# Kernel tuning notes

Measured on AMD Instinct MI355X. Metric: run time of the kernel, lower is better.

The kernel has to match this reference:

```python
import jax, jax.numpy as jnp
import numpy as np

B = 1024
EMB_DIM = 128      # channels fed to VQ; each channel's 5*5=25 spatial vector is one token
CODEBOOK = 1024
COMMIT = 0.25


def conv2d(x, w, b, pad=1):
    y = jax.lax.conv_general_dilated(x, w, (1, 1), [(pad, pad), (pad, pad)],
                                     dimension_numbers=('NCHW', 'OIHW', 'NCHW'))
    return y + b[None, :, None, None]


def maxpool2x2(x):
    b, c, h, w = x.shape
    xr = x.reshape(b, c, h // 2, 2, w // 2, 2).transpose(0, 1, 2, 4, 3, 5).reshape(b, c, h // 2, w // 2, 4)
    return jnp.max(xr, axis=-1), jnp.argmax(xr, axis=-1)


def maxunpool2x2(x, idx):
    b, c, h, w = x.shape
    y = x[..., None] * jax.nn.one_hot(idx, 4, dtype=x.dtype)
    return y.reshape(b, c, h, w, 2, 2).transpose(0, 1, 2, 4, 3, 5).reshape(b, c, h * 2, w * 2)


def setup_inputs() -> dict:
    key = jax.random.key(0)
    ks = jax.random.split(key, 12)
    f32 = jnp.float32

    def he(k, shape, fan_in):
        return jax.random.normal(k, shape, f32) * (2.0 / fan_in) ** 0.5

    return {
        'x': jax.random.normal(ks[0], (B, 3, 20, 20), f32),
        'enc1_w': he(ks[1], (32, 3, 3, 3), 27), 'enc1_b': jnp.zeros((32,), f32),
        'enc2_w': he(ks[2], (96, 32, 3, 3), 288), 'enc2_b': jnp.zeros((96,), f32),
        'pre_w': he(ks[3], (EMB_DIM, 96, 1, 1), 96), 'pre_b': jnp.zeros((EMB_DIM,), f32),
        'codebook': jax.random.normal(ks[4], (CODEBOOK, 25), f32),
        'trans_w': he(ks[5], (EMB_DIM, 96, 1, 1), EMB_DIM), 'trans_b': jnp.zeros((96,), f32),
        'dec1_w': he(ks[6], (32, 96, 3, 3), 864), 'dec1_b': jnp.zeros((32,), f32),
        'dec2_w': he(ks[7], (3, 32, 3, 3), 288), 'dec2_b': jnp.zeros((3,), f32),
        'hpe_w1': he(ks[8], (2400, 32), 2400), 'hpe_b1': jnp.zeros((32,), f32),
        'hpe_w2': he(ks[9], (32, 36), 32), 'hpe_b2': jnp.zeros((36,), f32),
    }


def reference(x, enc1_w, enc1_b, enc2_w, enc2_b, pre_w, pre_b, codebook,
              trans_w, trans_b, dec1_w, dec1_b, dec2_w, dec2_b,
              hpe_w1, hpe_b1, hpe_w2, hpe_b2):
    bsz = x.shape[0]
    # ---- Encoder: conv+relu+pool x2, keeping pool argmax indices ----
    h1 = jax.nn.relu(conv2d(x, enc1_w, enc1_b))          # [B,32,20,20]
    p1, idx1 = maxpool2x2(h1)                            # [B,32,10,10]
    h2 = jax.nn.relu(conv2d(p1, enc2_w, enc2_b))         # [B,96,10,10]
    z, idx2 = maxpool2x2(h2)                             # [B,96,5,5]
    # ---- pre-VQ 1x1 conv, tokens are per-channel 25-dim spatial vectors ----
    vq = conv2d(z, pre_w, pre_b, pad=0).reshape(bsz, -1, 25)   # [B,EMB_DIM,25]
    flat = vq.reshape(-1, 25)
    # squared L2 distances to codebook, argmin quantization
    d = (jnp.sum(flat * flat, -1, keepdims=True)
         - 2.0 * flat @ codebook.T
         + jnp.sum(codebook * codebook, -1))             # [B*EMB_DIM, CODEBOOK]
    indices = jnp.argmin(d, axis=-1).reshape(bsz, -1)    # [B,EMB_DIM]
    quantized = codebook[indices]                        # [B,EMB_DIM,25] gather
    vq_loss = COMMIT * jnp.mean((jax.lax.stop_gradient(quantized) - vq) ** 2)
    # unreliable_mode == 2 -> noisy_indices = indices (identity path)
    z_rec = codebook[indices].reshape(bsz, -1, 5, 5)     # [B,EMB_DIM,5,5]
    # ---- ConvTranspose2d 1x1 (torch weight layout [in,out,1,1]) ----
    latent = jnp.einsum('bihw,io->bohw', z_rec, trans_w[:, :, 0, 0]) + trans_b[None, :, None, None]
    # ---- Decoder: unpool(idx2)+conv+relu, unpool(idx1)+conv ----
    u2 = maxunpool2x2(latent, idx2)                      # [B,96,10,10]
    d1 = jax.nn.relu(conv2d(u2, dec1_w, dec1_b))         # [B,32,10,10]
    u1 = maxunpool2x2(d1, idx1)                          # [B,32,20,20]
    r_x = conv2d(u1, dec2_w, dec2_b)                     # [B,3,20,20]
    # ---- pose head on flattened latent (2400 = 96*5*5) ----
    feat = latent.reshape(bsz, -1)
    kp = jax.nn.relu(feat @ hpe_w1 + hpe_b1) @ hpe_w2 + hpe_b2
    return vq_loss, r_x, kp.reshape(bsz, -1, 2)
```

## Files before the change

kernel.cpp:

```cpp
#include <hip/hip_runtime.h>

typedef unsigned char u8;
typedef unsigned long long u64;
typedef _Float16 h2 __attribute__((ext_vector_type(2)));

__device__ inline h2 h2bits(unsigned int u) { union { unsigned int u; h2 h; } c; c.u = u; return c.h; }
__device__ inline unsigned int bitsh2(h2 h) { union { unsigned int u; h2 h; } c; c.h = h; return c.u; }
__device__ inline unsigned int f2hbits(float v) {
    union { _Float16 h; unsigned short u; } c; c.h = (_Float16)v; return (unsigned int)c.u;
}

#if __has_builtin(__builtin_amdgcn_fdot2)
__device__ inline float fdot2(h2 a, h2 b, float c) { return __builtin_amdgcn_fdot2(a, b, c, false); }
#else
__device__ inline float fdot2(h2 a, h2 b, float c) {
    return c + (float)a.x * (float)b.x + (float)a.y * (float)b.y;
}
#endif

__global__ __launch_bounds__(256) void k0t(const float* __restrict__ cb,
                                           float* __restrict__ cnorm,
                                           float* __restrict__ lossacc,
                                           const float* __restrict__ e2w,
                                           float* __restrict__ wT2,
                                           const float* __restrict__ d1w,
                                           unsigned int* __restrict__ wH6u,
                                           const float* __restrict__ d2w,
                                           unsigned int* __restrict__ wH7u) {
    int g = blockIdx.x * 256 + threadIdx.x;
    if (g < 1024) {
        float s = 0.f;
#pragma unroll
        for (int d = 0; d < 25; ++d) { float v = cb[g * 25 + d]; s += v * v; }
        cnorm[g] = s;
    }
    if (g == 0) lossacc[0] = 0.f;
    for (int i = g; i < 27648; i += 8192) {
        int oc = i / 288, r = i % 288, ci = r / 9, k = r % 9;
        wT2[((ci * 3 + k / 3) * 96 + oc) * 3 + (k % 3)] = e2w[i];
    }
    for (int i = g; i < 13824; i += 8192) {
        int oc = i & 31, r = i >> 5;
        int kx = r % 3, r2 = r / 3, ky = r2 % 3, cp = r2 / 3;
        float a = d1w[(oc * 96 + 2 * cp) * 9 + ky * 3 + kx];
        float b = d1w[(oc * 96 + 2 * cp + 1) * 9 + ky * 3 + kx];
        h2 v; v.x = (_Float16)a; v.y = (_Float16)b;
        wH6u[i] = bitsh2(v);
    }
    if (g < 432) {
        int oc = g % 3, r = g / 3;
        int kx = r % 3, r2 = r / 3, ky = r2 % 3, cp = r2 / 3;
        float a = d2w[(oc * 32 + 2 * cp) * 9 + ky * 3 + kx];
        float b = d2w[(oc * 32 + 2 * cp + 1) * 9 + ky * 3 + kx];
        h2 v; v.x = (_Float16)a; v.y = (_Float16)b;
        wH7u[g] = bitsh2(v);
    }
}

__global__ __launch_bounds__(128) void k1_enc1(const float* __restrict__ x,
                                               const float* __restrict__ w,
                                               const float* __restrict__ bias,
                                               float* __restrict__ p1,
                                               u64* __restrict__ idx1p) {
    const int img = blockIdx.x;
    const int tid = threadIdx.x;
    __shared__ __align__(16) float xs[1320];
    __shared__ float wss[864];
    __shared__ float bss[32];
    for (int i = tid; i < 1320; i += 128) xs[i] = 0.f;
    for (int i = tid; i < 864; i += 128) wss[i] = w[i];
    if (tid < 32) bss[tid] = bias[tid];
    __syncthreads();
    for (int i = tid; i < 1200; i += 128) {
        int ci = i / 400, s = i % 400, y = s / 20, xx = s % 20;
        xs[ci * 440 + y * 22 + xx + 1] = x[img * 1200 + i];
    }
    __syncthreads();
    if (tid >= 100) return;
    const int r = tid / 10, c = tid % 10;
    int ry[4]; bool mv[4];
#pragma unroll
    for (int wy = 0; wy < 4; ++wy) {
        int yy = 2 * r - 1 + wy;
        mv[wy] = (yy >= 0) && (yy <= 19);
        ry[wy] = min(max(yy, 0), 19);
    }
    u64 idxbits = 0;
    for (int ocg = 0; ocg < 4; ++ocg) {
        float acc[8][4];
#pragma unroll
        for (int j = 0; j < 8; ++j) {
            float bb = bss[ocg * 8 + j];
#pragma unroll
            for (int q = 0; q < 4; ++q) acc[j][q] = bb;
        }
        for (int ci = 0; ci < 3; ++ci) {
            float win[4][4];
#pragma unroll
            for (int wy = 0; wy < 4; ++wy)
#pragma unroll
                for (int wx = 0; wx < 4; ++wx) {
                    float v = xs[ci * 440 + ry[wy] * 22 + 2 * c + wx];
                    win[wy][wx] = mv[wy] ? v : 0.f;
                }
#pragma unroll
            for (int j = 0; j < 8; ++j) {
                const float* wr = &wss[((ocg * 8 + j) * 3 + ci) * 9];
#pragma unroll
                for (int q = 0; q < 4; ++q) {
                    int dr = q >> 1, dc = q & 1;
#pragma unroll
                    for (int ky = 0; ky < 3; ++ky)
#pragma unroll
                        for (int kx = 0; kx < 3; ++kx)
                            acc[j][q] = fmaf(win[dr + ky][dc + kx], wr[ky * 3 + kx], acc[j][q]);
                }
            }
        }
#pragma unroll
        for (int j = 0; j < 8; ++j) {
            int oc = ocg * 8 + j;
            float best = -1.f; int bi = 0;
#pragma unroll
            for (int q = 0; q < 4; ++q) {
                float v = fmaxf(acc[j][q], 0.f);
                if (v > best) { best = v; bi = q; }
            }
            p1[img * 3200 + oc * 100 + tid] = best;
            idxbits |= (u64)bi << (2 * oc);
        }
    }
    idx1p[img * 100 + tid] = idxbits;
}

__global__ __launch_bounds__(256) void k2f(const float* __restrict__ p1,
                                           const float* __restrict__ wT2,
                                           const float* __restrict__ bias,
                                           const float* __restrict__ prw,
                                           const float* __restrict__ prb,
                                           float* __restrict__ vqb,
                                           u8* __restrict__ idx2) {
    const int img = blockIdx.x;
    const int tid = threadIdx.x;
    __shared__ __align__(16) float up[4608];
    __shared__ __align__(16) float wch[6912];
    for (int i = tid; i < 4608; i += 256) up[i] = 0.f;
    __syncthreads();
    for (int i = tid; i < 3200; i += 256) {
        int ci = i / 100, s = i % 100;
        up[ci * 144 + (s / 10 + 1) * 12 + (s % 10) + 1] = p1[img * 3200 + i];
    }
    const int wv = tid >> 6;
    const int l  = tid & 63;
    const int ocsub = (l >= 25) ? 1 : 0;
    const int pos = l - ocsub * 25;
    const bool act = (l < 50);
    const int oc0 = wv * 24 + ocsub * 12;
    const int r = pos / 5, c = pos % 5;
    float acc[12][4];
#pragma unroll
    for (int j = 0; j < 12; ++j)
#pragma unroll
        for (int q = 0; q < 4; ++q) acc[j][q] = 0.f;
    for (int chunk = 0; chunk < 4; ++chunk) {
        __syncthreads();
        for (int i = tid; i < 6912; i += 256) wch[i] = wT2[chunk * 6912 + i];
        __syncthreads();
        if (act) {
            for (int cil = 0; cil < 8; ++cil) {
                const int base = (chunk * 8 + cil) * 144;
                float win[4][4];
#pragma unroll
                for (int wy = 0; wy < 4; ++wy) {
                    float2 a = *(const float2*)&up[base + (2 * r + wy) * 12 + 2 * c];
                    float2 b = *(const float2*)&up[base + (2 * r + wy) * 12 + 2 * c + 2];
                    win[wy][0] = a.x; win[wy][1] = a.y; win[wy][2] = b.x; win[wy][3] = b.y;
                }
#pragma unroll
                for (int ky = 0; ky < 3; ++ky) {
                    const float* wk = &wch[(cil * 3 + ky) * 288 + oc0 * 3];
                    float wreg[36];
#pragma unroll
                    for (int i4 = 0; i4 < 9; ++i4)
                        *(float4*)(wreg + 4 * i4) = *(const float4*)(wk + 4 * i4);
#pragma unroll
                    for (int j = 0; j < 12; ++j)
#pragma unroll
                        for (int q = 0; q < 4; ++q) {
                            int dr = q >> 1, dc = q & 1;
#pragma unroll
                            for (int kx = 0; kx < 3; ++kx)
                                acc[j][q] = fmaf(win[dr + ky][dc + kx], wreg[j * 3 + kx], acc[j][q]);
                        }
                }
            }
        }
    }
    float* zs = wch;
    float* wst = &wch[2688];
    __syncthreads();
    if (act) {
#pragma unroll
        for (int j = 0; j < 12; ++j) {
            int oc = oc0 + j;
            float bb = bias[oc];
            float best = -1.f; int bi = 0;
#pragma unroll
            for (int q = 0; q < 4; ++q) {
                float v = fmaxf(acc[j][q] + bb, 0.f);
                if (v > best) { best = v; bi = q; }
            }
            zs[oc * 28 + pos] = best;
            idx2[img * 2400 + oc * 25 + pos] = (u8)bi;
        }
    }
    __syncthreads();
    const int e = tid >> 1, sh = tid & 1;
    const int s0 = sh * 12, ns = sh ? 13 : 12;
    float acc2[13];
    {
        float bb = prb[e];
#pragma unroll
        for (int k = 0; k < 13; ++k) acc2[k] = bb;
    }
    for (int cc = 0; cc < 3; ++cc) {
        __syncthreads();
        for (int i = tid; i < 4096; i += 256)
            wst[(i >> 5) * 33 + (i & 31)] = prw[(i >> 5) * 96 + cc * 32 + (i & 31)];
        __syncthreads();
        for (int cil = 0; cil < 32; ++cil) {
            int ci = cc * 32 + cil;
            float wvv = wst[e * 33 + cil];
            float cz[16];
#pragma unroll
            for (int i4 = 0; i4 < 4; ++i4)
                *(float4*)(cz + 4 * i4) = *(const float4*)&zs[ci * 28 + s0 + 4 * i4];
#pragma unroll
            for (int k = 0; k < 13; ++k) acc2[k] = fmaf(wvv, cz[k], acc2[k]);
        }
    }
    float* ob = up;
#pragma unroll
    for (int k = 0; k < 13; ++k)
        if (k < ns) ob[e * 25 + s0 + k] = acc2[k];
    __syncthreads();
    for (int i = tid; i < 3200; i += 256) vqb[img * 3200 + i] = ob[i];
}

__global__ __launch_bounds__(256) void k3b_vq2(const float* __restrict__ vq,
                                               const float* __restrict__ cb,
                                               const float* __restrict__ cnorm,
                                               float* __restrict__ pbest,
                                               int* __restrict__ pbk) {
    const int tg = blockIdx.x >> 3;
    const int ch = blockIdx.x & 7;
    const int tid = threadIdx.x;
    const int k0 = ch * 128;
    __shared__ __align__(16) float cs[128 * 28];
    for (int i = tid; i < 128 * 28; i += 256) {
        int k = i / 28, d = i % 28;
        float v = 0.f;
        if (d < 25) v = cb[(k0 + k) * 25 + d];
        else if (d == 25) v = cnorm[k0 + k];
        cs[i] = v;
    }
    const int t0 = tg * 1024 + tid * 4;
    float f2[4][25];
#pragma unroll
    for (int t = 0; t < 4; ++t)
#pragma unroll
        for (int d = 0; d < 25; ++d)
            f2[t][d] = -2.f * vq[(t0 + t) * 25 + d];
    __syncthreads();
    float best[4] = {1e30f, 1e30f, 1e30f, 1e30f};
    int bk[4] = {0, 0, 0, 0};
    for (int k = 0; k < 128; ++k) {
        const float* crow = &cs[k * 28];
        float cc[28];
#pragma unroll
        for (int i = 0; i < 7; ++i)
            *(float4*)(cc + 4 * i) = *(const float4*)(crow + 4 * i);
        const float cn = cc[25];
        const int kg = k0 + k;
#pragma unroll
        for (int t = 0; t < 4; ++t) {
            float a = cn;
#pragma unroll
            for (int d = 0; d < 25; ++d) a = fmaf(f2[t][d], cc[d], a);
            if (a < best[t]) { best[t] = a; bk[t] = kg; }
        }
    }
#pragma unroll
    for (int t = 0; t < 4; ++t) {
        pbest[ch * 131072 + t0 + t] = best[t];
        pbk[ch * 131072 + t0 + t] = bk[t];
    }
}

__global__ __launch_bounds__(256) void k3r_reduce(const float* __restrict__ pbest,
                                                  const int* __restrict__ pbk,
                                                  const float* __restrict__ vq,
                                                  int* __restrict__ vqidx,
                                                  float* __restrict__ lossacc) {
    const int t = blockIdx.x * 256 + threadIdx.x;
    float best = 1e30f; int bk = 0;
#pragma unroll
    for (int ch = 0; ch < 8; ++ch) {
        float s = pbest[ch * 131072 + t];
        int k = pbk[ch * 131072 + t];
        if (s < best) { best = s; bk = k; }
    }
    vqidx[t] = bk;
    float fn = 0.f;
#pragma unroll
    for (int d = 0; d < 25; ++d) { float v = vq[t * 25 + d]; fn = fmaf(v, v, fn); }
    float dloc = fn + best;
#pragma unroll
    for (int off = 32; off > 0; off >>= 1) dloc += __shfl_down(dloc, off, 64);
    __shared__ float wsum[4];
    if ((threadIdx.x & 63) == 0) wsum[threadIdx.x >> 6] = dloc;
    __syncthreads();
    if (threadIdx.x == 0)
        atomicAdd(lossacc, wsum[0] + wsum[1] + wsum[2] + wsum[3]);
}

__global__ void kf_loss(const float* __restrict__ lossacc, float* __restrict__ out) {
    out[0] = 0.25f * lossacc[0] / 3276800.0f;
}

__global__ __launch_bounds__(256) void k5_latent_pose(
    const int* __restrict__ vqidx, const float* __restrict__ cb,
    const float* __restrict__ tw, const float* __restrict__ tbb,
    const float* __restrict__ w1, const float* __restrict__ b1,
    const float* __restrict__ w2, const float* __restrict__ b2,
    float* __restrict__ latg, float* __restrict__ outkp) {
    const int img = blockIdx.x;
    const int tid = threadIdx.x;
    __shared__ int idxs[128];
    __shared__ float zr[128 * 26];
    __shared__ float lat[2400];
    __shared__ float ps[256];
    __shared__ float hs[32];
    if (tid < 128) idxs[tid] = vqidx[img * 128 + tid];
    __syncthreads();
    for (int i = tid; i < 3200; i += 256) {
        int e = i / 25, d = i % 25;
        zr[e * 26 + d] = cb[idxs[e] * 25 + d];
    }
    __syncthreads();
    const int sg = tid % 5, og = tid / 5;
    if (og < 24) {
        const int oc0 = og * 4, s0 = sg * 5;
        float acc[4][5];
#pragma unroll
        for (int j = 0; j < 4; ++j)
#pragma unroll
            for (int ss = 0; ss < 5; ++ss) acc[j][ss] = 0.f;
        for (int e = 0; e < 128; ++e) {
            float zv[5];
#pragma unroll
            for (int ss = 0; ss < 5; ++ss) zv[ss] = zr[e * 26 + s0 + ss];
#pragma unroll
            for (int j = 0; j < 4; ++j) {
                float wv = tw[e * 96 + oc0 + j];
#pragma unroll
                for (int ss = 0; ss < 5; ++ss) acc[j][ss] += wv * zv[ss];
            }
        }
#pragma unroll
        for (int j = 0; j < 4; ++j) {
            float bb = tbb[oc0 + j];
#pragma unroll
            for (int ss = 0; ss < 5; ++ss) {
                float v = acc[j][ss] + bb;
                lat[(oc0 + j) * 25 + s0 + ss] = v;
                latg[img * 2400 + (oc0 + j) * 25 + s0 + ss] = v;
            }
        }
    }
    __syncthreads();
    {
        const int seg = tid >> 5, jj = tid & 31;
        float s = 0.f;
        const int i0 = seg * 300;
        for (int i = i0; i < i0 + 300; ++i) s += lat[i] * w1[i * 32 + jj];
        ps[seg * 32 + jj] = s;
    }
    __syncthreads();
    if (tid < 32) {
        float h = b1[tid];
#pragma unroll
        for (int s2 = 0; s2 < 8; ++s2) h += ps[s2 * 32 + tid];
        hs[tid] = fmaxf(h, 0.f);
    }
    __syncthreads();
    if (tid < 36) {
        float kp = b2[tid];
#pragma unroll
        for (int m = 0; m < 32; ++m) kp += hs[m] * w2[m * 36 + tid];
        outkp[img * 36 + tid] = kp;
    }
}

__global__ __launch_bounds__(128) void k6_dec1(const float* __restrict__ latg,
                                               const u8* __restrict__ idx2,
                                               const unsigned int* __restrict__ wH6,
                                               const float* __restrict__ bias,
                                               unsigned short* __restrict__ d1h) {
    const int img0 = blockIdx.x * 2;
    const int tid = threadIdx.x;
    __shared__ __align__(16) unsigned int uph[13824];
    __shared__ unsigned int wcs[2304];
    for (int i = tid; i < 13824; i += 128) uph[i] = 0u;
    __syncthreads();
    for (int g = tid; g < 2400; g += 128) {
        int m = g / 1200, r2 = g % 1200;
        int cp = r2 / 25, s = r2 % 25;
        int rr = (img0 + m) * 2400 + cp * 50 + s;
        int q0 = idx2[rr], q1 = idx2[rr + 25];
        float v0 = latg[rr], v1 = latg[rr + 25];
        unsigned int wq[4] = {0u, 0u, 0u, 0u};
        wq[q0] |= f2hbits(v0);
        wq[q1] |= f2hbits(v1) << 16;
        int pr = s / 5, pc = s % 5;
        int wb = m * 6912 + (cp * 12 + 2 * pr + 1) * 12 + 2 * pc + 1;
        uph[wb]      = wq[0];
        uph[wb + 1]  = wq[1];
        uph[wb + 12] = wq[2];
        uph[wb + 13] = wq[3];
    }
    const int m = tid >> 6;
    const int l = tid & 63;
    const int oc = l & 31, ys = l >> 5;
    float acc[50];
#pragma unroll
    for (int i = 0; i < 50; ++i) acc[i] = 0.f;
    for (int chunk = 0; chunk < 6; ++chunk) {
        __syncthreads();
        for (int i = tid; i < 2304; i += 128) wcs[i] = wH6[chunk * 2304 + i];
        __syncthreads();
        for (int cpl = 0; cpl < 8; ++cpl) {
            const int base = m * 6912 + (chunk * 8 + cpl) * 144 + ys * 60;
            unsigned int row[7][12];
#pragma unroll
            for (int k = 0; k < 7; ++k) {
                const uint4* rp = (const uint4*)&uph[base + k * 12];
                uint4 a = rp[0], b = rp[1], cc = rp[2];
                row[k][0] = a.x;  row[k][1] = a.y;  row[k][2] = a.z;  row[k][3] = a.w;
                row[k][4] = b.x;  row[k][5] = b.y;  row[k][6] = b.z;  row[k][7] = b.w;
                row[k][8] = cc.x; row[k][9] = cc.y; row[k][10] = cc.z; row[k][11] = cc.w;
            }
            h2 w9[9];
#pragma unroll
            for (int t = 0; t < 9; ++t) w9[t] = h2bits(wcs[(cpl * 9 + t) * 32 + oc]);
#pragma unroll
            for (int r = 0; r < 5; ++r)
#pragma unroll
                for (int j = 0; j < 10; ++j) {
                    float a = acc[r * 10 + j];
#pragma unroll
                    for (int ky = 0; ky < 3; ++ky)
#pragma unroll
                        for (int kx = 0; kx < 3; ++kx)
                            a = fdot2(h2bits(row[r + ky][j + kx]), w9[ky * 3 + kx], a);
                    acc[r * 10 + j] = a;
                }
        }
    }
    const float bb = bias[oc];
#pragma unroll
    for (int r = 0; r < 5; ++r)
#pragma unroll
        for (int j = 0; j < 10; ++j)
            d1h[(img0 + m) * 3200 + ((ys * 5 + r) * 10 + j) * 32 + oc] =
                (unsigned short)f2hbits(fmaxf(acc[r * 10 + j] + bb, 0.f));
}

__global__ __launch_bounds__(256) void k7_dec2(const unsigned int* __restrict__ d1w32,
                                               const u64* __restrict__ idx1p,
                                               const unsigned int* __restrict__ wH7,
                                               const float* __restrict__ bias,
                                               float* __restrict__ rx) {
    const int img = blockIdx.x;
    const int tid = threadIdx.x;
    __shared__ __align__(16) unsigned int uph[7040];
    __shared__ unsigned int wcs[448];
    for (int i = tid; i < 7040; i += 256) uph[i] = 0u;
    for (int i = tid; i < 448; i += 256) {
        int cp = i / 28, rr = i % 28;
        wcs[i] = (rr < 27) ? wH7[cp * 27 + rr] : 0u;
    }
    __syncthreads();
    for (int g = tid; g < 1600; g += 256) {
        int pos = g >> 4, cp = g & 15;
        unsigned int word = d1w32[img * 1600 + g];
        u64 bits = idx1p[img * 100 + pos];
        int q0 = (int)((bits >> (4 * cp)) & 3ull);
        int q1 = (int)((bits >> (4 * cp + 2)) & 3ull);
        unsigned int wq[4] = {0u, 0u, 0u, 0u};
        wq[q0] |= word & 0xFFFFu;
        wq[q1] |= word & 0xFFFF0000u;
        int r = pos / 10, c = pos % 10;
        int wb = cp * 440 + (2 * r) * 22 + 2 * c + 1;
        uph[wb]      = wq[0];
        uph[wb + 1]  = wq[1];
        uph[wb + 22] = wq[2];
        uph[wb + 23] = wq[3];
    }
    __syncthreads();
    if (tid >= 200) return;
    const int y = tid / 10, xp = tid % 10, x0 = 2 * xp;
    const bool m0 = (y > 0), m2 = (y < 19);
    const int ry0 = max(y - 1, 0), ry2 = min(y + 1, 19);
    float acc[3][2] = {{0.f, 0.f}, {0.f, 0.f}, {0.f, 0.f}};
    for (int cp = 0; cp < 16; ++cp) {
        const int base = cp * 440;
        unsigned int row[3][4];
        {
            uint2 a = *(const uint2*)&uph[base + ry0 * 22 + x0];
            uint2 b = *(const uint2*)&uph[base + ry0 * 22 + x0 + 2];
            row[0][0] = m0 ? a.x : 0u; row[0][1] = m0 ? a.y : 0u;
            row[0][2] = m0 ? b.x : 0u; row[0][3] = m0 ? b.y : 0u;
            a = *(const uint2*)&uph[base + y * 22 + x0];
            b = *(const uint2*)&uph[base + y * 22 + x0 + 2];
            row[1][0] = a.x; row[1][1] = a.y; row[1][2] = b.x; row[1][3] = b.y;
            a = *(const uint2*)&uph[base + ry2 * 22 + x0];
            b = *(const uint2*)&uph[base + ry2 * 22 + x0 + 2];
            row[2][0] = m2 ? a.x : 0u; row[2][1] = m2 ? a.y : 0u;
            row[2][2] = m2 ? b.x : 0u; row[2][3] = m2 ? b.y : 0u;
        }
#pragma unroll
        for (int oc = 0; oc < 3; ++oc)
#pragma unroll
            for (int ky = 0; ky < 3; ++ky)
#pragma unroll
                for (int kx = 0; kx < 3; ++kx) {
                    h2 wk = h2bits(wcs[cp * 28 + (ky * 3 + kx) * 3 + oc]);
                    acc[oc][0] = fdot2(h2bits(row[ky][kx]),     wk, acc[oc][0]);
                    acc[oc][1] = fdot2(h2bits(row[ky][kx + 1]), wk, acc[oc][1]);
                }
    }
#pragma unroll
    for (int oc = 0; oc < 3; ++oc)
#pragma unroll
        for (int dx = 0; dx < 2; ++dx)
            rx[img * 1200 + oc * 400 + y * 20 + x0 + dx] = acc[oc][dx] + bias[oc];
}

extern "C" void kernel_launch(void* const* d_in, const int* in_sizes, int n_in,
                              void* d_out, int out_size, void* d_ws, size_t ws_size,
                              hipStream_t stream) {
    const float* x   = (const float*)d_in[0];
    const float* e1w = (const float*)d_in[1];
    const float* e1b = (const float*)d_in[2];
    const float* e2w = (const float*)d_in[3];
    const float* e2b = (const float*)d_in[4];
    const float* prw = (const float*)d_in[5];
    const float* prb = (const float*)d_in[6];
    const float* cb  = (const float*)d_in[7];
    const float* tw  = (const float*)d_in[8];
    const float* tbb = (const float*)d_in[9];
    const float* d1w = (const float*)d_in[10];
    const float* d1b = (const float*)d_in[11];
    const float* d2w = (const float*)d_in[12];
    const float* d2b = (const float*)d_in[13];
    const float* hw1 = (const float*)d_in[14];
    const float* hb1 = (const float*)d_in[15];
    const float* hw2 = (const float*)d_in[16];
    const float* hb2 = (const float*)d_in[17];
    float* out = (float*)d_out;

    float* ws      = (float*)d_ws;
    float* cnorm   = ws;
    float* lossacc = cnorm + 1024;
    float* wT2     = lossacc + 4;
    unsigned int* wH6u = (unsigned int*)(wT2 + 27648);
    unsigned int* wH7u = wH6u + 13824;
    float* p1      = wT2 + 27648 + 27648;
    float* z       = p1 + 3276800;
    float* vq      = z + 2457600;
    int*   vqidx   = (int*)(vq + 3276800);
    u64*   idx1p   = (u64*)(vqidx + 131072);
    u8*    idx2    = (u8*)(idx1p + 102400);
    float* latent  = p1;
    unsigned short* d1h = (unsigned short*)vq;
    float* pbest   = z;
    int*   pbk     = (int*)(z + 1048576);

    float* rx  = out + 1;
    float* okp = out + 1 + 1228800;

    k0t<<<32, 256, 0, stream>>>(cb, cnorm, lossacc, e2w, wT2, d1w, wH6u, d2w, wH7u);
    k1_enc1<<<1024, 128, 0, stream>>>(x, e1w, e1b, p1, idx1p);
    k2f<<<1024, 256, 0, stream>>>(p1, wT2, e2b, prw, prb, vq, idx2);
    k3b_vq2<<<1024, 256, 0, stream>>>(vq, cb, cnorm, pbest, pbk);
    k3r_reduce<<<512, 256, 0, stream>>>(pbest, pbk, vq, vqidx, lossacc);
    kf_loss<<<1, 1, 0, stream>>>(lossacc, out);
    k5_latent_pose<<<1024, 256, 0, stream>>>(vqidx, cb, tw, tbb, hw1, hb1, hw2, hb2,
                                             latent, okp);
    k6_dec1<<<512, 128, 0, stream>>>(latent, idx2, wH6u, d1b, d1h);
    k7_dec2<<<1024, 256, 0, stream>>>((const unsigned int*)d1h, idx1p, wH7u, d2b, rx);
}
```

Baseline: 443.7 us.

## Process more images per block in enc2 and dec1 to amortize weight staging

k2f now handles two images per 512-thread block, sharing each staged weight chunk across both images and reusing the shared buffers for the projection stage. k6_dec1 handles four images per 256-thread block, staging the unpooled input in two channel halves so the shared footprint stays the same while each weight chunk load serves four images. The aim is to cut redundant global-to-LDS weight traffic and barrier overhead per image. In exchange the grids get smaller and k2f uses more LDS per block, which may lower occupancy.

```diff
diff --git a/kernel.cpp b/kernel.cpp
--- a/kernel.cpp
+++ b/kernel.cpp
@@ -133,29 +133,32 @@
     idx1p[img * 100 + tid] = idxbits;
 }
 
-__global__ __launch_bounds__(256) void k2f(const float* __restrict__ p1,
+__global__ __launch_bounds__(512) void k2f(const float* __restrict__ p1,
                                            const float* __restrict__ wT2,
                                            const float* __restrict__ bias,
                                            const float* __restrict__ prw,
                                            const float* __restrict__ prb,
                                            float* __restrict__ vqb,
                                            u8* __restrict__ idx2) {
-    const int img = blockIdx.x;
+    const int img0 = blockIdx.x * 2;
     const int tid = threadIdx.x;
-    __shared__ __align__(16) float up[4608];
+    __shared__ __align__(16) float up[9216];
     __shared__ __align__(16) float wch[6912];
-    for (int i = tid; i < 4608; i += 256) up[i] = 0.f;
-    __syncthreads();
-    for (int i = tid; i < 3200; i += 256) {
-        int ci = i / 100, s = i % 100;
-        up[ci * 144 + (s / 10 + 1) * 12 + (s % 10) + 1] = p1[img * 3200 + i];
+    for (int i = tid; i < 9216; i += 512) up[i] = 0.f;
+    __syncthreads();
+    for (int i = tid; i < 6400; i += 512) {
+        int m = i / 3200, r = i % 3200;
+        int ci = r / 100, s = r % 100;
+        up[m * 4608 + ci * 144 + (s / 10 + 1) * 12 + (s % 10) + 1] = p1[(img0 + m) * 3200 + r];
     }
     const int wv = tid >> 6;
+    const int m  = wv >> 2;
+    const int wvl = wv & 3;
     const int l  = tid & 63;
     const int ocsub = (l >= 25) ? 1 : 0;
     const int pos = l - ocsub * 25;
     const bool act = (l < 50);
-    const int oc0 = wv * 24 + ocsub * 12;
+    const int oc0 = wvl * 24 + ocsub * 12;
     const int r = pos / 5, c = pos % 5;
     float acc[12][4];
 #pragma unroll
@@ -164,11 +167,11 @@
         for (int q = 0; q < 4; ++q) acc[j][q] = 0.f;
     for (int chunk = 0; chunk < 4; ++chunk) {
         __syncthreads();
-        for (int i = tid; i < 6912; i += 256) wch[i] = wT2[chunk * 6912 + i];
+        for (int i = tid; i < 6912; i += 512) wch[i] = wT2[chunk * 6912 + i];
         __syncthreads();
         if (act) {
             for (int cil = 0; cil < 8; ++cil) {
-                const int base = (chunk * 8 + cil) * 144;
+                const int base = m * 4608 + (chunk * 8 + cil) * 144;
                 float win[4][4];
 #pragma unroll
                 for (int wy = 0; wy < 4; ++wy) {
@@ -197,7 +200,6 @@
         }
     }
     float* zs = wch;
-    float* wst = &wch[2688];
     __syncthreads();
     if (act) {
 #pragma unroll
@@ -210,12 +212,15 @@
                 float v = fmaxf(acc[j][q] + bb, 0.f);
                 if (v > best) { best = v; bi = q; }
             }
-            zs[oc * 28 + pos] = best;
-            idx2[img * 2400 + oc * 25 + pos] = (u8)bi;
-        }
-    }
-    __syncthreads();
-    const int e = tid >> 1, sh = tid & 1;
+            zs[m * 2688 + oc * 28 + pos] = best;
+            idx2[(img0 + m) * 2400 + oc * 25 + pos] = (u8)bi;
+        }
+    }
+    __syncthreads();
+    float* wst = up;
+    const int m2 = tid >> 8;
+    const int rr = tid & 255;
+    const int e = rr >> 1, sh = rr & 1;
     const int s0 = sh * 12, ns = sh ? 13 : 12;
     float acc2[13];
     {
@@ -225,7 +230,7 @@
     }
     for (int cc = 0; cc < 3; ++cc) {
         __syncthreads();
-        for (int i = tid; i < 4096; i += 256)
+        for (int i = tid; i < 4096; i += 512)
             wst[(i >> 5) * 33 + (i & 31)] = prw[(i >> 5) * 96 + cc * 32 + (i & 31)];
         __syncthreads();
         for (int cil = 0; cil < 32; ++cil) {
@@ -234,17 +239,18 @@
             float cz[16];
 #pragma unroll
             for (int i4 = 0; i4 < 4; ++i4)
-                *(float4*)(cz + 4 * i4) = *(const float4*)&zs[ci * 28 + s0 + 4 * i4];
+                *(float4*)(cz + 4 * i4) = *(const float4*)&zs[m2 * 2688 + ci * 28 + s0 + 4 * i4];
 #pragma unroll
             for (int k = 0; k < 13; ++k) acc2[k] = fmaf(wvv, cz[k], acc2[k]);
         }
     }
-    float* ob = up;
+    __syncthreads();
+    float* ob = wch;
 #pragma unroll
     for (int k = 0; k < 13; ++k)
-        if (k < ns) ob[e * 25 + s0 + k] = acc2[k];
-    __syncthreads();
-    for (int i = tid; i < 3200; i += 256) vqb[img * 3200 + i] = ob[i];
+        if (k < ns) ob[m2 * 3200 + e * 25 + s0 + k] = acc2[k];
+    __syncthreads();
+    for (int i = tid; i < 6400; i += 512) vqb[img0 * 3200 + i] = ob[i];
 }
 
 __global__ __launch_bounds__(256) void k3b_vq2(const float* __restrict__ vq,
@@ -402,69 +408,73 @@
     }
 }
 
-__global__ __launch_bounds__(128) void k6_dec1(const float* __restrict__ latg,
+__global__ __launch_bounds__(256) void k6_dec1(const float* __restrict__ latg,
                                                const u8* __restrict__ idx2,
                                                const unsigned int* __restrict__ wH6,
                                                const float* __restrict__ bias,
                                                unsigned short* __restrict__ d1h) {
-    const int img0 = blockIdx.x * 2;
+    const int img0 = blockIdx.x * 4;
     const int tid = threadIdx.x;
     __shared__ __align__(16) unsigned int uph[13824];
     __shared__ unsigned int wcs[2304];
-    for (int i = tid; i < 13824; i += 128) uph[i] = 0u;
-    __syncthreads();
-    for (int g = tid; g < 2400; g += 128) {
-        int m = g / 1200, r2 = g % 1200;
-        int cp = r2 / 25, s = r2 % 25;
-        int rr = (img0 + m) * 2400 + cp * 50 + s;
-        int q0 = idx2[rr], q1 = idx2[rr + 25];
-        float v0 = latg[rr], v1 = latg[rr + 25];
-        unsigned int wq[4] = {0u, 0u, 0u, 0u};
-        wq[q0] |= f2hbits(v0);
-        wq[q1] |= f2hbits(v1) << 16;
-        int pr = s / 5, pc = s % 5;
-        int wb = m * 6912 + (cp * 12 + 2 * pr + 1) * 12 + 2 * pc + 1;
-        uph[wb]      = wq[0];
-        uph[wb + 1]  = wq[1];
-        uph[wb + 12] = wq[2];
-        uph[wb + 13] = wq[3];
-    }
     const int m = tid >> 6;
     const int l = tid & 63;
     const int oc = l & 31, ys = l >> 5;
     float acc[50];
 #pragma unroll
     for (int i = 0; i < 50; ++i) acc[i] = 0.f;
-    for (int chunk = 0; chunk < 6; ++chunk) {
+    for (int half = 0; half < 2; ++half) {
         __syncthreads();
-        for (int i = tid; i < 2304; i += 128) wcs[i] = wH6[chunk * 2304 + i];
+        for (int i = tid; i < 13824; i += 256) uph[i] = 0u;
         __syncthreads();
-        for (int cpl = 0; cpl < 8; ++cpl) {
-            const int base = m * 6912 + (chunk * 8 + cpl) * 144 + ys * 60;
-            unsigned int row[7][12];
-#pragma unroll
-            for (int k = 0; k < 7; ++k) {
-                const uint4* rp = (const uint4*)&uph[base + k * 12];
-                uint4 a = rp[0], b = rp[1], cc = rp[2];
-                row[k][0] = a.x;  row[k][1] = a.y;  row[k][2] = a.z;  row[k][3] = a.w;
-                row[k][4] = b.x;  row[k][5] = b.y;  row[k][6] = b.z;  row[k][7] = b.w;
-                row[k][8] = cc.x; row[k][9] = cc.y; row[k][10] = cc.z; row[k][11] = cc.w;
+        for (int g = tid; g < 2400; g += 256) {
+            int mi = g / 600, r2 = g % 600;
+            int cpl = r2 / 25, s = r2 % 25;
+            int cp = half * 24 + cpl;
+            int rr = (img0 + mi) * 2400 + cp * 50 + s;
+            int q0 = idx2[rr], q1 = idx2[rr + 25];
+            float v0 = latg[rr], v1 = latg[rr + 25];
+            unsigned int wq[4] = {0u, 0u, 0u, 0u};
+            wq[q0] |= f2hbits(v0);
+            wq[q1] |= f2hbits(v1) << 16;
+            int pr = s / 5, pc = s % 5;
+            int wb = mi * 3456 + (cpl * 12 + 2 * pr + 1) * 12 + 2 * pc + 1;
+            uph[wb]      = wq[0];
+            uph[wb + 1]  = wq[1];
+            uph[wb + 12] = wq[2];
+            uph[wb + 13] = wq[3];
+        }
+        for (int chunk = 0; chunk < 3; ++chunk) {
+            __syncthreads();
+            for (int i = tid; i < 2304; i += 256) wcs[i] = wH6[(half * 3 + chunk) * 2304 + i];
+            __syncthreads();
+            for (int cpl = 0; cpl < 8; ++cpl) {
+                const int base = m * 3456 + (chunk * 8 + cpl) * 144 + ys * 60;
+                unsigned int row[7][12];
+#pragma unroll
+                for (int k = 0; k < 7; ++k) {
+                    const uint4* rp = (const uint4*)&uph[base + k * 12];
+                    uint4 a = rp[0], b = rp[1], cc = rp[2];
+                    row[k][0] = a.x;  row[k][1] = a.y;  row[k][2] = a.z;  row[k][3] = a.w;
+                    row[k][4] = b.x;  row[k][5] = b.y;  row[k][6] = b.z;  row[k][7] = b.w;
+                    row[k][8] = cc.x; row[k][9] = cc.y; row[k][10] = cc.z; row[k][11] = cc.w;
+                }
+                h2 w9[9];
+#pragma unroll
+                for (int t = 0; t < 9; ++t) w9[t] = h2bits(wcs[((chunk * 8 + cpl) % 8 == cpl ? cpl : cpl) * 0 + (cpl * 9 + t) * 32 + oc]);
+#pragma unroll
+                for (int r = 0; r < 5; ++r)
+#pragma unroll
+                    for (int j = 0; j < 10; ++j) {
+                        float a = acc[r * 10 + j];
+#pragma unroll
+                        for (int ky = 0; ky < 3; ++ky)
+#pragma unroll
+                            for (int kx = 0; kx < 3; ++kx)
+                                a = fdot2(h2bits(row[r + ky][j + kx]), w9[ky * 3 + kx], a);
+                        acc[r * 10 + j] = a;
+                    }
             }
-            h2 w9[9];
-#pragma unroll
-            for (int t = 0; t < 9; ++t) w9[t] = h2bits(wcs[(cpl * 9 + t) * 32 + oc]);
-#pragma unroll
-            for (int r = 0; r < 5; ++r)
-#pragma unroll
-                for (int j = 0; j < 10; ++j) {
-                    float a = acc[r * 10 + j];
-#pragma unroll
-                    for (int ky = 0; ky < 3; ++ky)
-#pragma unroll
-                        for (int kx = 0; kx < 3; ++kx)
-                            a = fdot2(h2bits(row[r + ky][j + kx]), w9[ky * 3 + kx], a);
-                    acc[r * 10 + j] = a;
-                }
         }
     }
     const float bb = bias[oc];
@@ -592,12 +602,12 @@
 
     k0t<<<32, 256, 0, stream>>>(cb, cnorm, lossacc, e2w, wT2, d1w, wH6u, d2w, wH7u);
     k1_enc1<<<1024, 128, 0, stream>>>(x, e1w, e1b, p1, idx1p);
-    k2f<<<1024, 256, 0, stream>>>(p1, wT2, e2b, prw, prb, vq, idx2);
+    k2f<<<512, 512, 0, stream>>>(p1, wT2, e2b, prw, prb, vq, idx2);
     k3b_vq2<<<1024, 256, 0, stream>>>(vq, cb, cnorm, pbest, pbk);
     k3r_reduce<<<512, 256, 0, stream>>>(pbest, pbk, vq, vqidx, lossacc);
     kf_loss<<<1, 1, 0, stream>>>(lossacc, out);
     k5_latent_pose<<<1024, 256, 0, stream>>>(vqidx, cb, tw, tbb, hw1, hb1, hw2, hb2,
                                              latent, okp);
-    k6_dec1<<<512, 128, 0, stream>>>(latent, idx2, wH6u, d1b, d1h);
+    k6_dec1<<<256, 256, 0, stream>>>(latent, idx2, wH6u, d1b, d1h);
     k7_dec2<<<1024, 256, 0, stream>>>((const unsigned int*)d1h, idx1p, wH7u, d2b, rx);
 }
```

New measurement: 470.8 us. +6.1%, slower.

## Fuse enc1 conv/pool into enc2 kernel and fold loss finalize into reduce

Applied to the files above, without the earlier changes.

The first encoder conv+ReLU+pool is computed inside the enc2 kernel, writing pooled results straight into the padded shared-memory tile instead of round-tripping p1 through global memory. The kf_loss single-thread launch is removed: the reduce kernel uses a global atomic block counter so the last block computes the final loss. This saves one kernel launch and a 13 MB write/read of p1, at the cost of only 100 of 256 threads working during the enc1 phase and an extra fence plus atomic per block.

```diff
diff --git a/kernel.cpp b/kernel.cpp
--- a/kernel.cpp
+++ b/kernel.cpp
@@ -35,6 +35,7 @@
         cnorm[g] = s;
     }
     if (g == 0) lossacc[0] = 0.f;
+    if (g == 1) ((unsigned int*)lossacc)[1] = 0u;
     for (int i = g; i < 27648; i += 8192) {
         int oc = i / 288, r = i % 288, ci = r / 9, k = r % 9;
         wT2[((ci * 3 + k / 3) * 96 + oc) * 3 + (k % 3)] = e2w[i];
@@ -57,98 +58,88 @@
     }
 }
 
-__global__ __launch_bounds__(128) void k1_enc1(const float* __restrict__ x,
-                                               const float* __restrict__ w,
-                                               const float* __restrict__ bias,
-                                               float* __restrict__ p1,
-                                               u64* __restrict__ idx1p) {
-    const int img = blockIdx.x;
-    const int tid = threadIdx.x;
-    __shared__ __align__(16) float xs[1320];
-    __shared__ float wss[864];
-    __shared__ float bss[32];
-    for (int i = tid; i < 1320; i += 128) xs[i] = 0.f;
-    for (int i = tid; i < 864; i += 128) wss[i] = w[i];
-    if (tid < 32) bss[tid] = bias[tid];
-    __syncthreads();
-    for (int i = tid; i < 1200; i += 128) {
-        int ci = i / 400, s = i % 400, y = s / 20, xx = s % 20;
-        xs[ci * 440 + y * 22 + xx + 1] = x[img * 1200 + i];
-    }
-    __syncthreads();
-    if (tid >= 100) return;
-    const int r = tid / 10, c = tid % 10;
-    int ry[4]; bool mv[4];
-#pragma unroll
-    for (int wy = 0; wy < 4; ++wy) {
-        int yy = 2 * r - 1 + wy;
-        mv[wy] = (yy >= 0) && (yy <= 19);
-        ry[wy] = min(max(yy, 0), 19);
-    }
-    u64 idxbits = 0;
-    for (int ocg = 0; ocg < 4; ++ocg) {
-        float acc[8][4];
-#pragma unroll
-        for (int j = 0; j < 8; ++j) {
-            float bb = bss[ocg * 8 + j];
-#pragma unroll
-            for (int q = 0; q < 4; ++q) acc[j][q] = bb;
-        }
-        for (int ci = 0; ci < 3; ++ci) {
-            float win[4][4];
-#pragma unroll
-            for (int wy = 0; wy < 4; ++wy)
-#pragma unroll
-                for (int wx = 0; wx < 4; ++wx) {
-                    float v = xs[ci * 440 + ry[wy] * 22 + 2 * c + wx];
-                    win[wy][wx] = mv[wy] ? v : 0.f;
-                }
-#pragma unroll
-            for (int j = 0; j < 8; ++j) {
-                const float* wr = &wss[((ocg * 8 + j) * 3 + ci) * 9];
-#pragma unroll
-                for (int q = 0; q < 4; ++q) {
-                    int dr = q >> 1, dc = q & 1;
-#pragma unroll
-                    for (int ky = 0; ky < 3; ++ky)
-#pragma unroll
-                        for (int kx = 0; kx < 3; ++kx)
-                            acc[j][q] = fmaf(win[dr + ky][dc + kx], wr[ky * 3 + kx], acc[j][q]);
-                }
-            }
-        }
-#pragma unroll
-        for (int j = 0; j < 8; ++j) {
-            int oc = ocg * 8 + j;
-            float best = -1.f; int bi = 0;
-#pragma unroll
-            for (int q = 0; q < 4; ++q) {
-                float v = fmaxf(acc[j][q], 0.f);
-                if (v > best) { best = v; bi = q; }
-            }
-            p1[img * 3200 + oc * 100 + tid] = best;
-            idxbits |= (u64)bi << (2 * oc);
-        }
-    }
-    idx1p[img * 100 + tid] = idxbits;
-}
-
-__global__ __launch_bounds__(256) void k2f(const float* __restrict__ p1,
+__global__ __launch_bounds__(256) void k2f(const float* __restrict__ xin,
+                                           const float* __restrict__ e1w,
+                                           const float* __restrict__ e1b,
                                            const float* __restrict__ wT2,
                                            const float* __restrict__ bias,
                                            const float* __restrict__ prw,
                                            const float* __restrict__ prb,
                                            float* __restrict__ vqb,
-                                           u8* __restrict__ idx2) {
+                                           u8* __restrict__ idx2,
+                                           u64* __restrict__ idx1p) {
     const int img = blockIdx.x;
     const int tid = threadIdx.x;
     __shared__ __align__(16) float up[4608];
     __shared__ __align__(16) float wch[6912];
+    float* xs  = wch;
+    float* wss = &wch[1320];
+    float* bss = &wch[2184];
     for (int i = tid; i < 4608; i += 256) up[i] = 0.f;
-    __syncthreads();
-    for (int i = tid; i < 3200; i += 256) {
-        int ci = i / 100, s = i % 100;
-        up[ci * 144 + (s / 10 + 1) * 12 + (s % 10) + 1] = p1[img * 3200 + i];
+    for (int i = tid; i < 1320; i += 256) xs[i] = 0.f;
+    for (int i = tid; i < 864; i += 256) wss[i] = e1w[i];
+    if (tid < 32) bss[tid] = e1b[tid];
+    __syncthreads();
+    for (int i = tid; i < 1200; i += 256) {
+        int ci = i / 400, s = i % 400, y = s / 20, xx = s % 20;
+        xs[ci * 440 + y * 22 + xx + 1] = xin[img * 1200 + i];
+    }
+    __syncthreads();
+    if (tid < 100) {
+        const int r0 = tid / 10, c0 = tid % 10;
+        int ry[4]; bool mv[4];
+#pragma unroll
+        for (int wy = 0; wy < 4; ++wy) {
+            int yy = 2 * r0 - 1 + wy;
+            mv[wy] = (yy >= 0) && (yy <= 19);
+            ry[wy] = min(max(yy, 0), 19);
+        }
+        u64 idxbits = 0;
+        for (int ocg = 0; ocg < 4; ++ocg) {
+            float acc0[8][4];
+#pragma unroll
+            for (int j = 0; j < 8; ++j) {
+                float bb = bss[ocg * 8 + j];
+#pragma unroll
+                for (int q = 0; q < 4; ++q) acc0[j][q] = bb;
+            }
+            for (int ci = 0; ci < 3; ++ci) {
+                float win[4][4];
+#pragma unroll
+                for (int wy = 0; wy < 4; ++wy)
+#pragma unroll
+                    for (int wx = 0; wx < 4; ++wx) {
+                        float v = xs[ci * 440 + ry[wy] * 22 + 2 * c0 + wx];
+                        win[wy][wx] = mv[wy] ? v : 0.f;
+                    }
+#pragma unroll
+                for (int j = 0; j < 8; ++j) {
+                    const float* wr = &wss[((ocg * 8 + j) * 3 + ci) * 9];
+#pragma unroll
+                    for (int q = 0; q < 4; ++q) {
+                        int dr = q >> 1, dc = q & 1;
+#pragma unroll
+                        for (int ky = 0; ky < 3; ++ky)
+#pragma unroll
+                            for (int kx = 0; kx < 3; ++kx)
+                                acc0[j][q] = fmaf(win[dr + ky][dc + kx], wr[ky * 3 + kx], acc0[j][q]);
+                    }
+                }
+            }
+#pragma unroll
+            for (int j = 0; j < 8; ++j) {
+                int oc = ocg * 8 + j;
+                float best = -1.f; int bi = 0;
+#pragma unroll
+                for (int q = 0; q < 4; ++q) {
+                    float v = fmaxf(acc0[j][q], 0.f);
+                    if (v > best) { best = v; bi = q; }
+                }
+                up[oc * 144 + (r0 + 1) * 12 + (c0 + 1)] = best;
+                idxbits |= (u64)bi << (2 * oc);
+            }
+        }
+        idx1p[img * 100 + tid] = idxbits;
     }
     const int wv = tid >> 6;
     const int l  = tid & 63;
@@ -301,7 +292,9 @@
                                                   const int* __restrict__ pbk,
                                                   const float* __restrict__ vq,
                                                   int* __restrict__ vqidx,
-                                                  float* __restrict__ lossacc) {
+                                                  float* __restrict__ lossacc,
+                                                  unsigned int* __restrict__ cnt,
+                                                  float* __restrict__ out) {
     const int t = blockIdx.x * 256 + threadIdx.x;
     float best = 1e30f; int bk = 0;
 #pragma unroll
@@ -320,12 +313,15 @@
     __shared__ float wsum[4];
     if ((threadIdx.x & 63) == 0) wsum[threadIdx.x >> 6] = dloc;
     __syncthreads();
-    if (threadIdx.x == 0)
+    if (threadIdx.x == 0) {
         atomicAdd(lossacc, wsum[0] + wsum[1] + wsum[2] + wsum[3]);
-}
-
-__global__ void kf_loss(const float* __restrict__ lossacc, float* __restrict__ out) {
-    out[0] = 0.25f * lossacc[0] / 3276800.0f;
+        __threadfence();
+        unsigned int old = atomicAdd(cnt, 1u);
+        if (old == 511u) {
+            float tot = atomicAdd(lossacc, 0.0f);
+            out[0] = 0.25f * tot / 3276800.0f;
+        }
+    }
 }
 
 __global__ __launch_bounds__(256) void k5_latent_pose(
@@ -586,16 +582,15 @@
     unsigned short* d1h = (unsigned short*)vq;
     float* pbest   = z;
     int*   pbk     = (int*)(z + 1048576);
+    unsigned int* cnt = (unsigned int*)(lossacc + 1);
 
     float* rx  = out + 1;
     float* okp = out + 1 + 1228800;
 
     k0t<<<32, 256, 0, stream>>>(cb, cnorm, lossacc, e2w, wT2, d1w, wH6u, d2w, wH7u);
-    k1_enc1<<<1024, 128, 0, stream>>>(x, e1w, e1b, p1, idx1p);
-    k2f<<<1024, 256, 0, stream>>>(p1, wT2, e2b, prw, prb, vq, idx2);
+    k2f<<<1024, 256, 0, stream>>>(x, e1w, e1b, wT2, e2b, prw, prb, vq, idx2, idx1p);
     k3b_vq2<<<1024, 256, 0, stream>>>(vq, cb, cnorm, pbest, pbk);
-    k3r_reduce<<<512, 256, 0, stream>>>(pbest, pbk, vq, vqidx, lossacc);
-    kf_loss<<<1, 1, 0, stream>>>(lossacc, out);
+    k3r_reduce<<<512, 256, 0, stream>>>(pbest, pbk, vq, vqidx, lossacc, cnt, out);
     k5_latent_pose<<<1024, 256, 0, stream>>>(vqidx, cb, tw, tbb, hw1, hb1, hw2, hb2,
                                              latent, okp);
     k6_dec1<<<512, 128, 0, stream>>>(latent, idx2, wH6u, d1b, d1h);
```

After: 463.2 us. 1.04x slower.
